# Kernel optimization log

Hardware: AMD Instinct MI355X
Metric: run time of the kernel (lower is better)

The kernel has to match this reference:

```python
import jax, jax.numpy as jnp
import numpy as np

B_, C_, H_, W_, N_ = 2, 256, 64, 64, 16


def setup_inputs() -> dict:
    key = jax.random.key(0)
    ks = jax.random.split(key, 6)
    return {
        "features": jax.random.normal(ks[0], (B_, C_, H_, W_), jnp.float32),
        "A_log": jax.random.normal(ks[1], (C_, N_), jnp.float32) * 0.5,
        "D": jax.random.normal(ks[2], (C_,), jnp.float32),
        "W_delta": jax.random.normal(ks[3], (C_, C_), jnp.float32) * 0.02,
        "b_delta": jnp.zeros((C_,), jnp.float32),
        "W_B": jax.random.normal(ks[4], (C_, N_), jnp.float32) * 0.02,
        "W_C": jax.random.normal(ks[5], (C_, N_), jnp.float32) * 0.02,
    }


def _selective_scan(x, A_log, D, W_delta, b_delta, W_B, W_C):
    # x: (B, L, C) -> (B, L, C). Canonical S6 selective scan (mamba corrector).
    delta = jax.nn.softplus(x @ W_delta + b_delta)          # (B, L, C)
    Bm = x @ W_B                                            # (B, L, N)
    Cm = x @ W_C                                            # (B, L, N)
    A = -jnp.exp(A_log)                                     # (C, N), negative real
    dA = jnp.exp(delta[..., None] * A)                      # (B, L, C, N)
    dBx = (delta * x)[..., None] * Bm[:, :, None, :]        # (B, L, C, N)

    def combine(left, right):
        a_l, b_l = left
        a_r, b_r = right
        return (a_l * a_r, a_r * b_l + b_r)

    # h_t = dA_t * h_{t-1} + dBx_t, computed in parallel over L
    _, h = jax.lax.associative_scan(combine, (dA, dBx), axis=1)
    y = jnp.einsum('blcn,bln->blc', h, Cm) + x * D          # (B, L, C)
    return y


def reference(features, A_log, D, W_delta, b_delta, W_B, W_C):
    B, C, H, W = features.shape
    corr = lambda x: _selective_scan(x, A_log, D, W_delta, b_delta, W_B, W_C)

    # direction 1: row-major forward
    flat = features.reshape(B, C, H * W).transpose(0, 2, 1)        # (B, HW, C)
    out1 = corr(flat)
    # direction 2: row-major reversed
    out2 = jnp.flip(corr(jnp.flip(flat, axis=1)), axis=1)
    # direction 3: rows flipped vertically (flip over H), scan, flip back
    rows = features.transpose(0, 2, 3, 1)                          # (B, H, W, C)
    rows_f = jnp.flip(rows, axis=1).reshape(B, H * W, C)
    out3 = jnp.flip(corr(rows_f).reshape(B, H, W, C), axis=1).reshape(B, H * W, C)
    # direction 4: column-major, flipped over W, scan, flip + transpose back
    cols = features.transpose(0, 3, 2, 1)                          # (B, W, H, C)
    cols_f = jnp.flip(cols, axis=1).reshape(B, W * H, C)
    out4 = jnp.flip(corr(cols_f).reshape(B, W, H, C), axis=1)
    out4 = out4.transpose(0, 2, 1, 3).reshape(B, H * W, C)

    mamba_out = (out1 + out2 + out3 + out4) / 4                    # (B, HW, C)
    return mamba_out.transpose(0, 2, 1).reshape(B, C, H, W)
```

## Files before the change

### kernel.cpp

```cpp
#include <hip/hip_runtime.h>
#include <cstdint>
#include <cstddef>

#define BB 2
#define CC 256
#define NN 16
#define LL 4096
#define NCH 128
#define CLEN 32
#define LOG2E 1.4426950408889634f

typedef __attribute__((ext_vector_type(8))) short short8;
typedef __attribute__((ext_vector_type(4))) float f32x4;

__device__ __forceinline__ float softplus_f(float z) {
    return fmaxf(z, 0.f) + log1pf(expf(-fabsf(z)));
}

__device__ __forceinline__ uint32_t pack_bf2(float d, float u) {
    uint32_t lo = (__float_as_uint(d) + 0x8000u) >> 16;
    uint32_t hh = (__float_as_uint(u) + 0x8000u) & 0xffff0000u;
    return hh | lo;
}

__device__ __forceinline__ short bf16r(float f) {
    return (short)((__float_as_uint(f) + 0x8000u) >> 16);
}

__global__ __launch_bounds__(256) void k1_mfma(
    const float* __restrict__ feat, const float* __restrict__ Wd,
    const float* __restrict__ bd, const float* __restrict__ WB,
    const float* __restrict__ WC, uint32_t* __restrict__ du,
    float* __restrict__ Bm, float* __restrict__ Cm)
{
    int blk = blockIdx.x;
    int b  = blk >> 9;
    int lt = (blk >> 2) & 127;
    int ct = blk & 3;
    int l0 = lt * 32, c0 = ct * 64;
    const float* fbase = feat + (size_t)b * CC * LL;
    int t    = threadIdx.x;
    int lane = t & 63;
    int wq   = t >> 6;
    int m    = lane & 15;
    int quad = lane >> 4;
    int m0   = (wq & 1) * 16;
    int n0   = (wq >> 1) * 32;
    bool doBC = (ct == 0);

    __shared__ __align__(16) short sA[32][264];
    __shared__ __align__(16) short sB[64][264];
    __shared__ __align__(16) short sWB[16][264];
    __shared__ __align__(16) short sWC[16][264];

    #pragma unroll
    for (int p = 0; p < 8; ++p) {
        int k  = p * 32 + (t >> 3);
        int lc = (t & 7) * 4;
        f32x4 v = *(const f32x4*)&fbase[(size_t)k * LL + l0 + lc];
        #pragma unroll
        for (int i = 0; i < 4; ++i) sA[lc + i][k] = bf16r(v[i]);
    }
    #pragma unroll
    for (int p = 0; p < 16; ++p) {
        int k  = p * 16 + (t >> 4);
        int cc = (t & 15) * 4;
        f32x4 v = *(const f32x4*)&Wd[(size_t)k * CC + c0 + cc];
        #pragma unroll
        for (int i = 0; i < 4; ++i) sB[cc + i][k] = bf16r(v[i]);
    }
    if (doBC) {
        #pragma unroll
        for (int p = 0; p < 4; ++p) {
            int k  = p * 64 + (t >> 2);
            int nc = (t & 3) * 4;
            f32x4 vb = *(const f32x4*)&WB[(size_t)k * NN + nc];
            f32x4 vc = *(const f32x4*)&WC[(size_t)k * NN + nc];
            #pragma unroll
            for (int i = 0; i < 4; ++i) {
                sWB[nc + i][k] = bf16r(vb[i]);
                sWC[nc + i][k] = bf16r(vc[i]);
            }
        }
    }
    __syncthreads();

    f32x4 acc0 = {0.f, 0.f, 0.f, 0.f};
    f32x4 acc1 = {0.f, 0.f, 0.f, 0.f};
    f32x4 accB = {0.f, 0.f, 0.f, 0.f};
    const short (*sWsel)[264] = (wq >> 1) ? sWC : sWB;

    for (int ks = 0; ks < 8; ++ks) {
        int k8 = ks * 32 + quad * 8;
        short8 af  = *(const short8*)&sA[m0 + m][k8];
        short8 bf0 = *(const short8*)&sB[n0 + m][k8];
        short8 bf1 = *(const short8*)&sB[n0 + 16 + m][k8];
        acc0 = __builtin_amdgcn_mfma_f32_16x16x32_bf16(af, bf0, acc0, 0, 0, 0);
        acc1 = __builtin_amdgcn_mfma_f32_16x16x32_bf16(af, bf1, acc1, 0, 0, 0);
        if (doBC) {
            short8 bbf = *(const short8*)&sWsel[m][k8];
            accB = __builtin_amdgcn_mfma_f32_16x16x32_bf16(af, bbf, accB, 0, 0, 0);
        }
    }

    if (doBC) {
        float* dst = (wq >> 1) ? Cm : Bm;
        #pragma unroll
        for (int r = 0; r < 4; ++r) {
            int l = l0 + m0 + quad * 4 + r;
            dst[((size_t)b * LL + l) * NN + m] = accB[r];
        }
    }

    float bd0 = bd[c0 + n0 + m];
    float bd1 = bd[c0 + n0 + 16 + m];
    int cA = c0 + n0 + m;
    int cB = cA + 16;
    int lb = l0 + m0 + quad * 4;
    f32x4 xv0 = *(const f32x4*)&fbase[(size_t)cA * LL + lb];
    f32x4 xv1 = *(const f32x4*)&fbase[(size_t)cB * LL + lb];
    #pragma unroll
    for (int r = 0; r < 4; ++r) {
        float d0 = softplus_f(acc0[r] + bd0);
        float d1 = softplus_f(acc1[r] + bd1);
        du[((size_t)b * LL + lb + r) * CC + cA] = pack_bf2(d0, d0 * xv0[r]);
        du[((size_t)b * LL + lb + r) * CC + cB] = pack_bf2(d1, d1 * xv1[r]);
    }
}

__global__ __launch_bounds__(256) void p1_aggr(
    const uint32_t* __restrict__ du, const float* __restrict__ Bm,
    const float* __restrict__ A_log, float* __restrict__ P, float* __restrict__ S)
{
    int blk = blockIdx.x;
    int b  = (blk >> 7) & 1;
    int ch = blk & 127;
    int c = threadIdx.x;
    __shared__ float sBm[CLEN * NN];
    __shared__ uint32_t sW[CLEN * 256];

    float A2[NN];
    {
        const float4* al = (const float4*)(A_log + c * NN);
        #pragma unroll
        for (int q = 0; q < 4; ++q) {
            float4 v = al[q];
            A2[q*4+0] = -expf(v.x) * LOG2E;
            A2[q*4+1] = -expf(v.y) * LOG2E;
            A2[q*4+2] = -expf(v.z) * LOG2E;
            A2[q*4+3] = -expf(v.w) * LOG2E;
        }
    }

    if (blk < 256) {
        int p0 = 32 * ch;
        for (int i = threadIdx.x; i < CLEN * NN; i += 256) {
            int j = i >> 4, nn = i & 15;
            sBm[i] = Bm[((size_t)b * LL + (p0 + j)) * NN + nn];
        }
        const uint32_t* dub = du + (size_t)b * LL * CC + c;
        {
            uint32_t wt[CLEN];
            #pragma unroll
            for (int j = 0; j < CLEN; ++j) wt[j] = dub[(size_t)(p0 + j) * CC];
            #pragma unroll
            for (int j = 0; j < CLEN; ++j) sW[j * 256 + c] = wt[j];
        }
        __syncthreads();
        float Sf[NN] = {}, Sr[NN] = {}, pref[NN];
        #pragma unroll
        for (int nn = 0; nn < NN; ++nn) pref[nn] = 1.f;
        float sumd = 0.f;
        #pragma unroll 1
        for (int j = 0; j < CLEN; ++j) {
            uint32_t wj = sW[j * 256 + c];
            float dx = __uint_as_float(wj << 16);
            float uy = __uint_as_float(wj & 0xffff0000u);
            sumd += dx;
            float dA[NN];
            #pragma unroll
            for (int nn = 0; nn < NN; ++nn) dA[nn] = __builtin_amdgcn_exp2f(A2[nn] * dx);
            #pragma unroll
            for (int nn = 0; nn < NN; ++nn) {
                float Bu = uy * sBm[j * 16 + nn];
                Sf[nn] = fmaf(dA[nn], Sf[nn], Bu);
                Sr[nn] = fmaf(pref[nn], Bu, Sr[nn]);
                pref[nn] *= dA[nn];
            }
        }
        size_t base0 = ((size_t)(b * 128 + ch)) * 4096 + (size_t)c * 16;
        size_t base1 = ((size_t)((2 + b) * 128 + (127 - ch))) * 4096 + (size_t)c * 16;
        #pragma unroll
        for (int nn = 0; nn < NN; ++nn) {
            P[base0 + nn] = __builtin_amdgcn_exp2f(A2[nn] * sumd);
            S[base0 + nn] = Sf[nn];
            S[base1 + nn] = Sr[nn];
        }
    } else {
        int p0 = 63 - (ch >> 1) + 2048 * (ch & 1);
        const int inner = 64;
        for (int i = threadIdx.x; i < CLEN * NN; i += 256) {
            int j = i >> 4, nn = i & 15;
            sBm[i] = Bm[((size_t)b * LL + (p0 + inner * j)) * NN + nn];
        }
        const uint32_t* dub = du + (size_t)b * LL * CC + c;
        {
            uint32_t wt[CLEN];
            #pragma unroll
            for (int j = 0; j < CLEN; ++j) wt[j] = dub[(size_t)(p0 + inner * j) * CC];
            #pragma unroll
            for (int j = 0; j < CLEN; ++j) sW[j * 256 + c] = wt[j];
        }
        __syncthreads();
        float Sv[NN] = {};
        float sumd = 0.f;
        #pragma unroll 1
        for (int j = 0; j < CLEN; ++j) {
            uint32_t wj = sW[j * 256 + c];
            float dx = __uint_as_float(wj << 16);
            float uy = __uint_as_float(wj & 0xffff0000u);
            sumd += dx;
            float dA[NN];
            #pragma unroll
            for (int nn = 0; nn < NN; ++nn) dA[nn] = __builtin_amdgcn_exp2f(A2[nn] * dx);
            #pragma unroll
            for (int nn = 0; nn < NN; ++nn)
                Sv[nn] = fmaf(dA[nn], Sv[nn], uy * sBm[j * 16 + nn]);
        }
        size_t base = ((size_t)((4 + b) * 128 + ch)) * 4096 + (size_t)c * 16;
        #pragma unroll
        for (int nn = 0; nn < NN; ++nn) {
            P[base + nn] = __builtin_amdgcn_exp2f(A2[nn] * sumd);
            S[base + nn] = Sv[nn];
        }
    }
}

__global__ __launch_bounds__(128) void p2_scan(
    const float* __restrict__ P, const float* __restrict__ S, float* __restrict__ Hin)
{
    int r = blockIdx.x * 128 + threadIdx.x;
    int cn = r & 4095;
    int db = r >> 12;
    int d = db >> 1;
    int cls = (d == 1) ? 1 : ((d == 3) ? 2 : 0);
    int b = db & 1;
    const size_t sbase = ((size_t)(cls * 2 + b) * 128) * 4096 + cn;
    const size_t pbase = (d == 1) ? (((size_t)b * 128) * 4096 + cn) : sbase;
    const size_t obase = ((size_t)db * 128) * 4096 + cn;
    float h = 0.f;
    for (int g = 0; g < 16; ++g) {
        float pv[8], sv[8];
        #pragma unroll
        for (int i = 0; i < 8; ++i) {
            int ch = g * 8 + i;
            int chm = (d == 2) ? (126 - 2 * (ch >> 1) + (ch & 1)) : ch;
            int chp = (d == 1) ? (127 - ch) : chm;
            pv[i] = P[pbase + (size_t)chp * 4096];
            sv[i] = S[sbase + (size_t)chm * 4096];
        }
        #pragma unroll
        for (int i = 0; i < 8; ++i) {
            Hin[obase + (size_t)(g * 8 + i) * 4096] = h;
            h = fmaf(pv[i], h, sv[i]);
        }
    }
}

__global__ __launch_bounds__(256) void p3_replay(
    const uint32_t* __restrict__ du, const float* __restrict__ Bm,
    const float* __restrict__ Cm, const float* __restrict__ A_log,
    const float* __restrict__ Hin, float* __restrict__ yAB,
    float* __restrict__ yC)
{
    int blk = blockIdx.x;
    int b  = (blk >> 7) & 1;
    int ch = blk & 127;
    int c = threadIdx.x;
    __shared__ float sBm[CLEN * NN];
    __shared__ float sCm[CLEN * NN];
    __shared__ uint32_t sW[CLEN * 256];
    __shared__ float sY[CLEN * 256];

    float A2[NN];
    {
        const float4* al = (const float4*)(A_log + c * NN);
        #pragma unroll
        for (int q = 0; q < 4; ++q) {
            float4 v = al[q];
            A2[q*4+0] = -expf(v.x) * LOG2E;
            A2[q*4+1] = -expf(v.y) * LOG2E;
            A2[q*4+2] = -expf(v.z) * LOG2E;
            A2[q*4+3] = -expf(v.w) * LOG2E;
        }
    }

    if (blk < 256) {
        int p0 = 32 * ch;
        for (int i = threadIdx.x; i < CLEN * NN; i += 256) {
            int j = i >> 4, nn = i & 15;
            size_t o = ((size_t)b * LL + (p0 + j)) * NN + nn;
            sBm[i] = Bm[o];
            sCm[i] = Cm[o];
        }
        const uint32_t* dub = du + (size_t)b * LL * CC + c;
        {
            uint32_t wt[CLEN];
            #pragma unroll
            for (int j = 0; j < CLEN; ++j) wt[j] = dub[(size_t)(p0 + j) * CC];
            #pragma unroll
            for (int j = 0; j < CLEN; ++j) sW[j * 256 + c] = wt[j];
        }

        int chr = 127 - ch;
        float h1[NN];
        {
            const float4* hp1 = (const float4*)(Hin + ((size_t)(1 * 2 + b) * 128 + chr) * 4096 + (size_t)c * 16);
            #pragma unroll
            for (int q = 0; q < 4; ++q) {
                float4 v1 = hp1[q];
                h1[q*4+0]=v1.x; h1[q*4+1]=v1.y; h1[q*4+2]=v1.z; h1[q*4+3]=v1.w;
            }
        }
        __syncthreads();
        #pragma unroll 1
        for (int j = CLEN - 1; j >= 0; --j) {
            uint32_t wj = sW[j * 256 + c];
            float dx = __uint_as_float(wj << 16);
            float uy = __uint_as_float(wj & 0xffff0000u);
            float dA[NN];
            #pragma unroll
            for (int nn = 0; nn < NN; ++nn) dA[nn] = __builtin_amdgcn_exp2f(A2[nn] * dx);
            float yv = 0.f;
            #pragma unroll
            for (int nn = 0; nn < NN; ++nn) {
                float Bu = uy * sBm[j * 16 + nn];
                h1[nn] = fmaf(dA[nn], h1[nn], Bu);
                yv = fmaf(h1[nn], sCm[j * 16 + nn], yv);
            }
            sY[j * 256 + c] = yv;
        }

        int ch2 = 126 - (ch & ~1) + (ch & 1);
        float h0[NN], h2[NN];
        {
            const float4* hp0 = (const float4*)(Hin + ((size_t)(0 * 2 + b) * 128 + ch)  * 4096 + (size_t)c * 16);
            const float4* hp2 = (const float4*)(Hin + ((size_t)(2 * 2 + b) * 128 + ch2) * 4096 + (size_t)c * 16);
            #pragma unroll
            for (int q = 0; q < 4; ++q) {
                float4 v0 = hp0[q], v2 = hp2[q];
                h0[q*4+0]=v0.x; h0[q*4+1]=v0.y; h0[q*4+2]=v0.z; h0[q*4+3]=v0.w;
                h2[q*4+0]=v2.x; h2[q*4+1]=v2.y; h2[q*4+2]=v2.z; h2[q*4+3]=v2.w;
            }
        }
        #pragma unroll 1
        for (int j = 0; j < CLEN; ++j) {
            uint32_t wj = sW[j * 256 + c];
            float dx = __uint_as_float(wj << 16);
            float uy = __uint_as_float(wj & 0xffff0000u);
            float dA[NN];
            #pragma unroll
            for (int nn = 0; nn < NN; ++nn) dA[nn] = __builtin_amdgcn_exp2f(A2[nn] * dx);
            float y0v = 0.f, y2v = 0.f;
            #pragma unroll
            for (int nn = 0; nn < NN; ++nn) {
                float Bu = uy * sBm[j * 16 + nn];
                float cm = sCm[j * 16 + nn];
                h0[nn] = fmaf(dA[nn], h0[nn], Bu);
                h2[nn] = fmaf(dA[nn], h2[nn], Bu);
                y0v = fmaf(h0[nn], cm, y0v);
                y2v = fmaf(h2[nn], cm, y2v);
            }
            yAB[((size_t)b * LL + p0 + j) * CC + c] = 0.25f * (y0v + y2v + sY[j * 256 + c]);
        }
    } else {
        int p0 = 63 - (ch >> 1) + 2048 * (ch & 1);
        const int inner = 64;
        for (int i = threadIdx.x; i < CLEN * NN; i += 256) {
            int j = i >> 4, nn = i & 15;
            size_t o = ((size_t)b * LL + (p0 + inner * j)) * NN + nn;
            sBm[i] = Bm[o];
            sCm[i] = Cm[o];
        }
        const uint32_t* dub = du + (size_t)b * LL * CC + c;
        {
            uint32_t wt[CLEN];
            #pragma unroll
            for (int j = 0; j < CLEN; ++j) wt[j] = dub[(size_t)(p0 + inner * j) * CC];
            #pragma unroll
            for (int j = 0; j < CLEN; ++j) sW[j * 256 + c] = wt[j];
        }
        float h[NN];
        {
            const float4* hp = (const float4*)(Hin + ((size_t)(3 * 2 + b) * 128 + ch) * 4096 + (size_t)c * 16);
            #pragma unroll
            for (int q = 0; q < 4; ++q) {
                float4 v = hp[q];
                h[q*4+0]=v.x; h[q*4+1]=v.y; h[q*4+2]=v.z; h[q*4+3]=v.w;
            }
        }
        __syncthreads();
        #pragma unroll 1
        for (int j = 0; j < CLEN; ++j) {
            uint32_t wj = sW[j * 256 + c];
            float dx = __uint_as_float(wj << 16);
            float uy = __uint_as_float(wj & 0xffff0000u);
            float dA[NN];
            #pragma unroll
            for (int nn = 0; nn < NN; ++nn) dA[nn] = __builtin_amdgcn_exp2f(A2[nn] * dx);
            float yv = 0.f;
            #pragma unroll
            for (int nn = 0; nn < NN; ++nn) {
                float Bu = uy * sBm[j * 16 + nn];
                h[nn] = fmaf(dA[nn], h[nn], Bu);
                yv = fmaf(h[nn], sCm[j * 16 + nn], yv);
            }
            yC[((size_t)b * LL + p0 + inner * j) * CC + c] = 0.25f * yv;
        }
    }
}

__global__ __launch_bounds__(256) void k6_reduce(
    const float* __restrict__ feat, const float* __restrict__ D,
    const float* __restrict__ yAB, const float* __restrict__ yC,
    float* __restrict__ out)
{
    int pt = blockIdx.x & 63;
    int ct = (blockIdx.x >> 6) & 3;
    int b  = blockIdx.x >> 8;
    int p0 = pt * 64, c0 = ct * 64;
    __shared__ float tile[64 * 65];
    {
        int cl = threadIdx.x & 63;
        int pg = threadIdx.x >> 6;
        #pragma unroll
        for (int pp = 0; pp < 16; ++pp) {
            int pl = pp * 4 + pg;
            size_t ix = ((size_t)b * LL + p0 + pl) * CC + c0 + cl;
            tile[cl * 65 + pl] = yAB[ix] + yC[ix];
        }
    }
    __syncthreads();
    {
        int pl = threadIdx.x & 63;
        int cg = threadIdx.x >> 6;
        #pragma unroll
        for (int cc = 0; cc < 16; ++cc) {
            int cloc = cc * 4 + cg;
            int c = c0 + cloc;
            size_t o = ((size_t)b * CC + c) * LL + p0 + pl;
            out[o] = tile[cloc * 65 + pl] + feat[o] * D[c];
        }
    }
}

extern "C" void kernel_launch(void* const* d_in, const int* in_sizes, int n_in,
                              void* d_out, int out_size, void* d_ws, size_t ws_size,
                              hipStream_t stream)
{
    const float* feat  = (const float*)d_in[0];
    const float* A_log = (const float*)d_in[1];
    const float* D     = (const float*)d_in[2];
    const float* Wd    = (const float*)d_in[3];
    const float* bd    = (const float*)d_in[4];
    const float* WB    = (const float*)d_in[5];
    const float* WC    = (const float*)d_in[6];
    float* out = (float*)d_out;

    float* ws  = (float*)d_ws;
    uint32_t* du = (uint32_t*)ws;
    float* Bm  = ws  + (size_t)2097152;
    float* Cm  = Bm  + (size_t)131072;
    float* P   = Cm  + (size_t)131072;
    float* S   = P   + (size_t)3145728;
    float* Hin = S   + (size_t)3145728;
    float* yAB = Hin + (size_t)4194304;
    float* yC  = yAB + (size_t)2097152;

    k1_mfma<<<1024, 256, 0, stream>>>(feat, Wd, bd, WB, WC, du, Bm, Cm);
    p1_aggr<<<512, 256, 0, stream>>>(du, Bm, A_log, P, S);
    p2_scan<<<256, 128, 0, stream>>>(P, S, Hin);
    p3_replay<<<512, 256, 0, stream>>>(du, Bm, Cm, A_log, Hin, yAB, yC);
    k6_reduce<<<512, 256, 0, stream>>>(feat, D, yAB, yC, out);
}
```

Baseline: 153.5 us.

## Fuse all five stages into one persistent kernel with grid barriers

Replaces the five separate launches (projection GEMM, chunk aggregation, inter-chunk scan, replay, reduce) with a single persistent kernel of 512 blocks. The stages are separated by atomic-counter grid barriers, with a memset to reset the counters before launch. The aggregation and replay stages now reuse the same shared-memory chunk data, so the du/Bm/Cm reload in the replay stage is removed. The aim is to remove launch gaps and the redundant reload. In exchange, all 512 blocks must be co-resident to avoid deadlock, the spin barriers add their own cost, and the scan stage uses only part of the grid.

```diff
diff --git a/kernel.cpp b/kernel.cpp
--- a/kernel.cpp
+++ b/kernel.cpp
@@ -2,12 +2,11 @@
 #include <cstdint>
 #include <cstddef>
 
-#define BB 2
 #define CC 256
 #define NN 16
 #define LL 4096
-#define NCH 128
 #define CLEN 32
+#define NBLK 512
 #define LOG2E 1.4426950408889634f
 
 typedef __attribute__((ext_vector_type(8))) short short8;
@@ -27,18 +26,37 @@
     return (short)((__float_as_uint(f) + 0x8000u) >> 16);
 }
 
-__global__ __launch_bounds__(256) void k1_mfma(
-    const float* __restrict__ feat, const float* __restrict__ Wd,
+__device__ __forceinline__ void gbar(uint32_t* cnt) {
+    __syncthreads();
+    if (threadIdx.x == 0) {
+        __threadfence();
+        atomicAdd(cnt, 1u);
+        int spins = 0;
+        while (atomicAdd(cnt, 0u) < (uint32_t)NBLK) {
+            __builtin_amdgcn_s_sleep(16);
+            if (++spins > (1 << 26)) break;
+        }
+        __threadfence();
+    }
+    __syncthreads();
+}
+
+union Smem {
+    struct { short A[32][264]; short B[64][264]; short WB[16][264]; short WC[16][264]; } k1;
+    struct { float bm[CLEN * NN]; float cm[CLEN * NN]; uint32_t w[CLEN * 256]; float y[CLEN * 256]; } ps;
+    float tile[64 * 65];
+};
+
+__global__ __launch_bounds__(256, 2) void fused_all(
+    const float* __restrict__ feat, const float* __restrict__ A_log,
+    const float* __restrict__ Dv, const float* __restrict__ Wd,
     const float* __restrict__ bd, const float* __restrict__ WB,
-    const float* __restrict__ WC, uint32_t* __restrict__ du,
-    float* __restrict__ Bm, float* __restrict__ Cm)
+    const float* __restrict__ WC, float* __restrict__ out,
+    uint32_t* __restrict__ du, float* __restrict__ Bm, float* __restrict__ Cm,
+    float* __restrict__ P, float* __restrict__ S, float* __restrict__ Hin,
+    float* __restrict__ yAB, float* __restrict__ yC, uint32_t* __restrict__ bar)
 {
-    int blk = blockIdx.x;
-    int b  = blk >> 9;
-    int lt = (blk >> 2) & 127;
-    int ct = blk & 3;
-    int l0 = lt * 32, c0 = ct * 64;
-    const float* fbase = feat + (size_t)b * CC * LL;
+    __shared__ Smem sm;
     int t    = threadIdx.x;
     int lane = t & 63;
     int wq   = t >> 6;
@@ -46,99 +64,92 @@
     int quad = lane >> 4;
     int m0   = (wq & 1) * 16;
     int n0   = (wq >> 1) * 32;
-    bool doBC = (ct == 0);
-
-    __shared__ __align__(16) short sA[32][264];
-    __shared__ __align__(16) short sB[64][264];
-    __shared__ __align__(16) short sWB[16][264];
-    __shared__ __align__(16) short sWC[16][264];
-
-    #pragma unroll
-    for (int p = 0; p < 8; ++p) {
-        int k  = p * 32 + (t >> 3);
-        int lc = (t & 7) * 4;
-        f32x4 v = *(const f32x4*)&fbase[(size_t)k * LL + l0 + lc];
-        #pragma unroll
-        for (int i = 0; i < 4; ++i) sA[lc + i][k] = bf16r(v[i]);
-    }
-    #pragma unroll
-    for (int p = 0; p < 16; ++p) {
-        int k  = p * 16 + (t >> 4);
-        int cc = (t & 15) * 4;
-        f32x4 v = *(const f32x4*)&Wd[(size_t)k * CC + c0 + cc];
-        #pragma unroll
-        for (int i = 0; i < 4; ++i) sB[cc + i][k] = bf16r(v[i]);
-    }
-    if (doBC) {
-        #pragma unroll
-        for (int p = 0; p < 4; ++p) {
-            int k  = p * 64 + (t >> 2);
-            int nc = (t & 3) * 4;
-            f32x4 vb = *(const f32x4*)&WB[(size_t)k * NN + nc];
-            f32x4 vc = *(const f32x4*)&WC[(size_t)k * NN + nc];
-            #pragma unroll
-            for (int i = 0; i < 4; ++i) {
-                sWB[nc + i][k] = bf16r(vb[i]);
-                sWC[nc + i][k] = bf16r(vc[i]);
-            }
-        }
-    }
-    __syncthreads();
-
-    f32x4 acc0 = {0.f, 0.f, 0.f, 0.f};
-    f32x4 acc1 = {0.f, 0.f, 0.f, 0.f};
-    f32x4 accB = {0.f, 0.f, 0.f, 0.f};
-    const short (*sWsel)[264] = (wq >> 1) ? sWC : sWB;
-
-    for (int ks = 0; ks < 8; ++ks) {
-        int k8 = ks * 32 + quad * 8;
-        short8 af  = *(const short8*)&sA[m0 + m][k8];
-        short8 bf0 = *(const short8*)&sB[n0 + m][k8];
-        short8 bf1 = *(const short8*)&sB[n0 + 16 + m][k8];
-        acc0 = __builtin_amdgcn_mfma_f32_16x16x32_bf16(af, bf0, acc0, 0, 0, 0);
-        acc1 = __builtin_amdgcn_mfma_f32_16x16x32_bf16(af, bf1, acc1, 0, 0, 0);
+
+    for (int it = 0; it < 2; ++it) {
+        __syncthreads();
+        int blk = it * 512 + blockIdx.x;
+        int b  = blk >> 9;
+        int lt = (blk >> 2) & 127;
+        int ct = blk & 3;
+        int l0 = lt * 32, c0 = ct * 64;
+        const float* fbase = feat + (size_t)b * CC * LL;
+        bool doBC = (ct == 0);
+
+        #pragma unroll
+        for (int p = 0; p < 8; ++p) {
+            int k  = p * 32 + (t >> 3);
+            int lc = (t & 7) * 4;
+            f32x4 v = *(const f32x4*)&fbase[(size_t)k * LL + l0 + lc];
+            #pragma unroll
+            for (int i = 0; i < 4; ++i) sm.k1.A[lc + i][k] = bf16r(v[i]);
+        }
+        #pragma unroll
+        for (int p = 0; p < 16; ++p) {
+            int k  = p * 16 + (t >> 4);
+            int cc = (t & 15) * 4;
+            f32x4 v = *(const f32x4*)&Wd[(size_t)k * CC + c0 + cc];
+            #pragma unroll
+            for (int i = 0; i < 4; ++i) sm.k1.B[cc + i][k] = bf16r(v[i]);
+        }
         if (doBC) {
-            short8 bbf = *(const short8*)&sWsel[m][k8];
-            accB = __builtin_amdgcn_mfma_f32_16x16x32_bf16(af, bbf, accB, 0, 0, 0);
-        }
-    }
-
-    if (doBC) {
-        float* dst = (wq >> 1) ? Cm : Bm;
+            #pragma unroll
+            for (int p = 0; p < 4; ++p) {
+                int k  = p * 64 + (t >> 2);
+                int nc = (t & 3) * 4;
+                f32x4 vb = *(const f32x4*)&WB[(size_t)k * NN + nc];
+                f32x4 vc = *(const f32x4*)&WC[(size_t)k * NN + nc];
+                #pragma unroll
+                for (int i = 0; i < 4; ++i) {
+                    sm.k1.WB[nc + i][k] = bf16r(vb[i]);
+                    sm.k1.WC[nc + i][k] = bf16r(vc[i]);
+                }
+            }
+        }
+        __syncthreads();
+
+        f32x4 acc0 = {0.f, 0.f, 0.f, 0.f};
+        f32x4 acc1 = {0.f, 0.f, 0.f, 0.f};
+        f32x4 accB = {0.f, 0.f, 0.f, 0.f};
+        const short (*sWsel)[264] = (wq >> 1) ? sm.k1.WC : sm.k1.WB;
+        for (int ks = 0; ks < 8; ++ks) {
+            int k8 = ks * 32 + quad * 8;
+            short8 af  = *(const short8*)&sm.k1.A[m0 + m][k8];
+            short8 bf0 = *(const short8*)&sm.k1.B[n0 + m][k8];
+            short8 bf1 = *(const short8*)&sm.k1.B[n0 + 16 + m][k8];
+            acc0 = __builtin_amdgcn_mfma_f32_16x16x32_bf16(af, bf0, acc0, 0, 0, 0);
+            acc1 = __builtin_amdgcn_mfma_f32_16x16x32_bf16(af, bf1, acc1, 0, 0, 0);
+            if (doBC) {
+                short8 bbf = *(const short8*)&sWsel[m][k8];
+                accB = __builtin_amdgcn_mfma_f32_16x16x32_bf16(af, bbf, accB, 0, 0, 0);
+            }
+        }
+        if (doBC) {
+            float* dst = (wq >> 1) ? Cm : Bm;
+            #pragma unroll
+            for (int r = 0; r < 4; ++r) {
+                int l = l0 + m0 + quad * 4 + r;
+                dst[((size_t)b * LL + l) * NN + m] = accB[r];
+            }
+        }
+        float bd0 = bd[c0 + n0 + m];
+        float bd1 = bd[c0 + n0 + 16 + m];
+        int cA = c0 + n0 + m;
+        int cB = cA + 16;
+        int lb = l0 + m0 + quad * 4;
+        f32x4 xv0 = *(const f32x4*)&fbase[(size_t)cA * LL + lb];
+        f32x4 xv1 = *(const f32x4*)&fbase[(size_t)cB * LL + lb];
         #pragma unroll
         for (int r = 0; r < 4; ++r) {
-            int l = l0 + m0 + quad * 4 + r;
-            dst[((size_t)b * LL + l) * NN + m] = accB[r];
-        }
-    }
-
-    float bd0 = bd[c0 + n0 + m];
-    float bd1 = bd[c0 + n0 + 16 + m];
-    int cA = c0 + n0 + m;
-    int cB = cA + 16;
-    int lb = l0 + m0 + quad * 4;
-    f32x4 xv0 = *(const f32x4*)&fbase[(size_t)cA * LL + lb];
-    f32x4 xv1 = *(const f32x4*)&fbase[(size_t)cB * LL + lb];
-    #pragma unroll
-    for (int r = 0; r < 4; ++r) {
-        float d0 = softplus_f(acc0[r] + bd0);
-        float d1 = softplus_f(acc1[r] + bd1);
-        du[((size_t)b * LL + lb + r) * CC + cA] = pack_bf2(d0, d0 * xv0[r]);
-        du[((size_t)b * LL + lb + r) * CC + cB] = pack_bf2(d1, d1 * xv1[r]);
-    }
-}
-
-__global__ __launch_bounds__(256) void p1_aggr(
-    const uint32_t* __restrict__ du, const float* __restrict__ Bm,
-    const float* __restrict__ A_log, float* __restrict__ P, float* __restrict__ S)
-{
-    int blk = blockIdx.x;
-    int b  = (blk >> 7) & 1;
-    int ch = blk & 127;
-    int c = threadIdx.x;
-    __shared__ float sBm[CLEN * NN];
-    __shared__ uint32_t sW[CLEN * 256];
-
+            float d0 = softplus_f(acc0[r] + bd0);
+            float d1 = softplus_f(acc1[r] + bd1);
+            du[((size_t)b * LL + lb + r) * CC + cA] = pack_bf2(d0, d0 * xv0[r]);
+            du[((size_t)b * LL + lb + r) * CC + cB] = pack_bf2(d1, d1 * xv1[r]);
+        }
+    }
+
+    gbar(bar + 0);
+
+    int c = t;
     float A2[NN];
     {
         const float4* al = (const float4*)(A_log + c * NN);
@@ -152,28 +163,38 @@
         }
     }
 
-    if (blk < 256) {
-        int p0 = 32 * ch;
-        for (int i = threadIdx.x; i < CLEN * NN; i += 256) {
-            int j = i >> 4, nn = i & 15;
-            sBm[i] = Bm[((size_t)b * LL + (p0 + j)) * NN + nn];
-        }
-        const uint32_t* dub = du + (size_t)b * LL * CC + c;
-        {
-            uint32_t wt[CLEN];
-            #pragma unroll
-            for (int j = 0; j < CLEN; ++j) wt[j] = dub[(size_t)(p0 + j) * CC];
-            #pragma unroll
-            for (int j = 0; j < CLEN; ++j) sW[j * 256 + c] = wt[j];
-        }
-        __syncthreads();
+    int blk = blockIdx.x;
+    int b1  = (blk >> 7) & 1;
+    int ch  = blk & 127;
+    bool isRow = (blk < 256);
+    int p0, inner;
+    if (isRow) { p0 = 32 * ch;                              inner = 1;  }
+    else       { p0 = 63 - (ch >> 1) + 2048 * (ch & 1);     inner = 64; }
+
+    for (int i = t; i < CLEN * NN; i += 256) {
+        int j = i >> 4, nn = i & 15;
+        size_t o = ((size_t)b1 * LL + (p0 + inner * j)) * NN + nn;
+        sm.ps.bm[i] = Bm[o];
+        sm.ps.cm[i] = Cm[o];
+    }
+    {
+        const uint32_t* dub = du + (size_t)b1 * LL * CC + c;
+        uint32_t wt[CLEN];
+        #pragma unroll
+        for (int j = 0; j < CLEN; ++j) wt[j] = dub[(size_t)(p0 + inner * j) * CC];
+        #pragma unroll
+        for (int j = 0; j < CLEN; ++j) sm.ps.w[j * 256 + c] = wt[j];
+    }
+    __syncthreads();
+
+    if (isRow) {
         float Sf[NN] = {}, Sr[NN] = {}, pref[NN];
         #pragma unroll
         for (int nn = 0; nn < NN; ++nn) pref[nn] = 1.f;
         float sumd = 0.f;
         #pragma unroll 1
         for (int j = 0; j < CLEN; ++j) {
-            uint32_t wj = sW[j * 256 + c];
+            uint32_t wj = sm.ps.w[j * 256 + c];
             float dx = __uint_as_float(wj << 16);
             float uy = __uint_as_float(wj & 0xffff0000u);
             sumd += dx;
@@ -182,14 +203,14 @@
             for (int nn = 0; nn < NN; ++nn) dA[nn] = __builtin_amdgcn_exp2f(A2[nn] * dx);
             #pragma unroll
             for (int nn = 0; nn < NN; ++nn) {
-                float Bu = uy * sBm[j * 16 + nn];
+                float Bu = uy * sm.ps.bm[j * 16 + nn];
                 Sf[nn] = fmaf(dA[nn], Sf[nn], Bu);
                 Sr[nn] = fmaf(pref[nn], Bu, Sr[nn]);
                 pref[nn] *= dA[nn];
             }
         }
-        size_t base0 = ((size_t)(b * 128 + ch)) * 4096 + (size_t)c * 16;
-        size_t base1 = ((size_t)((2 + b) * 128 + (127 - ch))) * 4096 + (size_t)c * 16;
+        size_t base0 = ((size_t)(b1 * 128 + ch)) * 4096 + (size_t)c * 16;
+        size_t base1 = ((size_t)((2 + b1) * 128 + (127 - ch))) * 4096 + (size_t)c * 16;
         #pragma unroll
         for (int nn = 0; nn < NN; ++nn) {
             P[base0 + nn] = __builtin_amdgcn_exp2f(A2[nn] * sumd);
@@ -197,26 +218,11 @@
             S[base1 + nn] = Sr[nn];
         }
     } else {
-        int p0 = 63 - (ch >> 1) + 2048 * (ch & 1);
-        const int inner = 64;
-        for (int i = threadIdx.x; i < CLEN * NN; i += 256) {
-            int j = i >> 4, nn = i & 15;
-            sBm[i] = Bm[((size_t)b * LL + (p0 + inner * j)) * NN + nn];
-        }
-        const uint32_t* dub = du + (size_t)b * LL * CC + c;
-        {
-            uint32_t wt[CLEN];
-            #pragma unroll
-            for (int j = 0; j < CLEN; ++j) wt[j] = dub[(size_t)(p0 + inner * j) * CC];
-            #pragma unroll
-            for (int j = 0; j < CLEN; ++j) sW[j * 256 + c] = wt[j];
-        }
-        __syncthreads();
         float Sv[NN] = {};
         float sumd = 0.f;
         #pragma unroll 1
         for (int j = 0; j < CLEN; ++j) {
-            uint32_t wj = sW[j * 256 + c];
+            uint32_t wj = sm.ps.w[j * 256 + c];
             float dx = __uint_as_float(wj << 16);
             float uy = __uint_as_float(wj & 0xffff0000u);
             sumd += dx;
@@ -225,107 +231,65 @@
             for (int nn = 0; nn < NN; ++nn) dA[nn] = __builtin_amdgcn_exp2f(A2[nn] * dx);
             #pragma unroll
             for (int nn = 0; nn < NN; ++nn)
-                Sv[nn] = fmaf(dA[nn], Sv[nn], uy * sBm[j * 16 + nn]);
-        }
-        size_t base = ((size_t)((4 + b) * 128 + ch)) * 4096 + (size_t)c * 16;
+                Sv[nn] = fmaf(dA[nn], Sv[nn], uy * sm.ps.bm[j * 16 + nn]);
+        }
+        size_t base = ((size_t)((4 + b1) * 128 + ch)) * 4096 + (size_t)c * 16;
         #pragma unroll
         for (int nn = 0; nn < NN; ++nn) {
             P[base + nn] = __builtin_amdgcn_exp2f(A2[nn] * sumd);
             S[base + nn] = Sv[nn];
         }
     }
-}
-
-__global__ __launch_bounds__(128) void p2_scan(
-    const float* __restrict__ P, const float* __restrict__ S, float* __restrict__ Hin)
-{
-    int r = blockIdx.x * 128 + threadIdx.x;
-    int cn = r & 4095;
-    int db = r >> 12;
-    int d = db >> 1;
-    int cls = (d == 1) ? 1 : ((d == 3) ? 2 : 0);
-    int b = db & 1;
-    const size_t sbase = ((size_t)(cls * 2 + b) * 128) * 4096 + cn;
-    const size_t pbase = (d == 1) ? (((size_t)b * 128) * 4096 + cn) : sbase;
-    const size_t obase = ((size_t)db * 128) * 4096 + cn;
-    float h = 0.f;
-    for (int g = 0; g < 16; ++g) {
-        float pv[8], sv[8];
-        #pragma unroll
-        for (int i = 0; i < 8; ++i) {
-            int ch = g * 8 + i;
-            int chm = (d == 2) ? (126 - 2 * (ch >> 1) + (ch & 1)) : ch;
-            int chp = (d == 1) ? (127 - ch) : chm;
-            pv[i] = P[pbase + (size_t)chp * 4096];
-            sv[i] = S[sbase + (size_t)chm * 4096];
-        }
-        #pragma unroll
-        for (int i = 0; i < 8; ++i) {
-            Hin[obase + (size_t)(g * 8 + i) * 4096] = h;
-            h = fmaf(pv[i], h, sv[i]);
-        }
-    }
-}
-
-__global__ __launch_bounds__(256) void p3_replay(
-    const uint32_t* __restrict__ du, const float* __restrict__ Bm,
-    const float* __restrict__ Cm, const float* __restrict__ A_log,
-    const float* __restrict__ Hin, float* __restrict__ yAB,
-    float* __restrict__ yC)
-{
-    int blk = blockIdx.x;
-    int b  = (blk >> 7) & 1;
-    int ch = blk & 127;
-    int c = threadIdx.x;
-    __shared__ float sBm[CLEN * NN];
-    __shared__ float sCm[CLEN * NN];
-    __shared__ uint32_t sW[CLEN * 256];
-    __shared__ float sY[CLEN * 256];
-
-    float A2[NN];
+
+    gbar(bar + 1);
+
     {
-        const float4* al = (const float4*)(A_log + c * NN);
-        #pragma unroll
-        for (int q = 0; q < 4; ++q) {
-            float4 v = al[q];
-            A2[q*4+0] = -expf(v.x) * LOG2E;
-            A2[q*4+1] = -expf(v.y) * LOG2E;
-            A2[q*4+2] = -expf(v.z) * LOG2E;
-            A2[q*4+3] = -expf(v.w) * LOG2E;
-        }
-    }
-
-    if (blk < 256) {
-        int p0 = 32 * ch;
-        for (int i = threadIdx.x; i < CLEN * NN; i += 256) {
-            int j = i >> 4, nn = i & 15;
-            size_t o = ((size_t)b * LL + (p0 + j)) * NN + nn;
-            sBm[i] = Bm[o];
-            sCm[i] = Cm[o];
-        }
-        const uint32_t* dub = du + (size_t)b * LL * CC + c;
-        {
-            uint32_t wt[CLEN];
-            #pragma unroll
-            for (int j = 0; j < CLEN; ++j) wt[j] = dub[(size_t)(p0 + j) * CC];
-            #pragma unroll
-            for (int j = 0; j < CLEN; ++j) sW[j * 256 + c] = wt[j];
-        }
-
+        int gid = blockIdx.x * 256 + t;
+        if (gid < 32768) {
+            int cn = gid & 4095;
+            int db = gid >> 12;
+            int d = db >> 1;
+            int cls = (d == 1) ? 1 : ((d == 3) ? 2 : 0);
+            int bb = db & 1;
+            const size_t sbase = ((size_t)(cls * 2 + bb) * 128) * 4096 + cn;
+            const size_t pbase = (d == 1) ? (((size_t)bb * 128) * 4096 + cn) : sbase;
+            const size_t obase = ((size_t)db * 128) * 4096 + cn;
+            float h = 0.f;
+            for (int g = 0; g < 16; ++g) {
+                float pv[8], sv[8];
+                #pragma unroll
+                for (int i = 0; i < 8; ++i) {
+                    int cc = g * 8 + i;
+                    int chm = (d == 2) ? (126 - 2 * (cc >> 1) + (cc & 1)) : cc;
+                    int chp = (d == 1) ? (127 - cc) : chm;
+                    pv[i] = P[pbase + (size_t)chp * 4096];
+                    sv[i] = S[sbase + (size_t)chm * 4096];
+                }
+                #pragma unroll
+                for (int i = 0; i < 8; ++i) {
+                    Hin[obase + (size_t)(g * 8 + i) * 4096] = h;
+                    h = fmaf(pv[i], h, sv[i]);
+                }
+            }
+        }
+    }
+
+    gbar(bar + 2);
+
+    if (isRow) {
         int chr = 127 - ch;
         float h1[NN];
         {
-            const float4* hp1 = (const float4*)(Hin + ((size_t)(1 * 2 + b) * 128 + chr) * 4096 + (size_t)c * 16);
+            const float4* hp1 = (const float4*)(Hin + ((size_t)(1 * 2 + b1) * 128 + chr) * 4096 + (size_t)c * 16);
             #pragma unroll
             for (int q = 0; q < 4; ++q) {
                 float4 v1 = hp1[q];
                 h1[q*4+0]=v1.x; h1[q*4+1]=v1.y; h1[q*4+2]=v1.z; h1[q*4+3]=v1.w;
             }
         }
-        __syncthreads();
         #pragma unroll 1
         for (int j = CLEN - 1; j >= 0; --j) {
-            uint32_t wj = sW[j * 256 + c];
+            uint32_t wj = sm.ps.w[j * 256 + c];
             float dx = __uint_as_float(wj << 16);
             float uy = __uint_as_float(wj & 0xffff0000u);
             float dA[NN];
@@ -334,18 +298,17 @@
             float yv = 0.f;
             #pragma unroll
             for (int nn = 0; nn < NN; ++nn) {
-                float Bu = uy * sBm[j * 16 + nn];
+                float Bu = uy * sm.ps.bm[j * 16 + nn];
                 h1[nn] = fmaf(dA[nn], h1[nn], Bu);
-                yv = fmaf(h1[nn], sCm[j * 16 + nn], yv);
-            }
-            sY[j * 256 + c] = yv;
-        }
-
+                yv = fmaf(h1[nn], sm.ps.cm[j * 16 + nn], yv);
+            }
+            sm.ps.y[j * 256 + c] = yv;
+        }
         int ch2 = 126 - (ch & ~1) + (ch & 1);
         float h0[NN], h2[NN];
         {
-            const float4* hp0 = (const float4*)(Hin + ((size_t)(0 * 2 + b) * 128 + ch)  * 4096 + (size_t)c * 16);
-            const float4* hp2 = (const float4*)(Hin + ((size_t)(2 * 2 + b) * 128 + ch2) * 4096 + (size_t)c * 16);
+            const float4* hp0 = (const float4*)(Hin + ((size_t)(0 * 2 + b1) * 128 + ch)  * 4096 + (size_t)c * 16);
+            const float4* hp2 = (const float4*)(Hin + ((size_t)(2 * 2 + b1) * 128 + ch2) * 4096 + (size_t)c * 16);
             #pragma unroll
             for (int q = 0; q < 4; ++q) {
                 float4 v0 = hp0[q], v2 = hp2[q];
@@ -355,7 +318,7 @@
         }
         #pragma unroll 1
         for (int j = 0; j < CLEN; ++j) {
-            uint32_t wj = sW[j * 256 + c];
+            uint32_t wj = sm.ps.w[j * 256 + c];
             float dx = __uint_as_float(wj << 16);
             float uy = __uint_as_float(wj & 0xffff0000u);
             float dA[NN];
@@ -364,45 +327,28 @@
             float y0v = 0.f, y2v = 0.f;
             #pragma unroll
             for (int nn = 0; nn < NN; ++nn) {
-                float Bu = uy * sBm[j * 16 + nn];
-                float cm = sCm[j * 16 + nn];
+                float Bu = uy * sm.ps.bm[j * 16 + nn];
+                float cm = sm.ps.cm[j * 16 + nn];
                 h0[nn] = fmaf(dA[nn], h0[nn], Bu);
                 h2[nn] = fmaf(dA[nn], h2[nn], Bu);
                 y0v = fmaf(h0[nn], cm, y0v);
                 y2v = fmaf(h2[nn], cm, y2v);
             }
-            yAB[((size_t)b * LL + p0 + j) * CC + c] = 0.25f * (y0v + y2v + sY[j * 256 + c]);
+            yAB[((size_t)b1 * LL + p0 + j) * CC + c] = 0.25f * (y0v + y2v + sm.ps.y[j * 256 + c]);
         }
     } else {
-        int p0 = 63 - (ch >> 1) + 2048 * (ch & 1);
-        const int inner = 64;
-        for (int i = threadIdx.x; i < CLEN * NN; i += 256) {
-            int j = i >> 4, nn = i & 15;
-            size_t o = ((size_t)b * LL + (p0 + inner * j)) * NN + nn;
-            sBm[i] = Bm[o];
-            sCm[i] = Cm[o];
-        }
-        const uint32_t* dub = du + (size_t)b * LL * CC + c;
-        {
-            uint32_t wt[CLEN];
-            #pragma unroll
-            for (int j = 0; j < CLEN; ++j) wt[j] = dub[(size_t)(p0 + inner * j) * CC];
-            #pragma unroll
-            for (int j = 0; j < CLEN; ++j) sW[j * 256 + c] = wt[j];
-        }
         float h[NN];
         {
-            const float4* hp = (const float4*)(Hin + ((size_t)(3 * 2 + b) * 128 + ch) * 4096 + (size_t)c * 16);
+            const float4* hp = (const float4*)(Hin + ((size_t)(3 * 2 + b1) * 128 + ch) * 4096 + (size_t)c * 16);
             #pragma unroll
             for (int q = 0; q < 4; ++q) {
                 float4 v = hp[q];
                 h[q*4+0]=v.x; h[q*4+1]=v.y; h[q*4+2]=v.z; h[q*4+3]=v.w;
             }
         }
-        __syncthreads();
         #pragma unroll 1
         for (int j = 0; j < CLEN; ++j) {
-            uint32_t wj = sW[j * 256 + c];
+            uint32_t wj = sm.ps.w[j * 256 + c];
             float dx = __uint_as_float(wj << 16);
             float uy = __uint_as_float(wj & 0xffff0000u);
             float dA[NN];
@@ -411,45 +357,42 @@
             float yv = 0.f;
             #pragma unroll
             for (int nn = 0; nn < NN; ++nn) {
-                float Bu = uy * sBm[j * 16 + nn];
+                float Bu = uy * sm.ps.bm[j * 16 + nn];
                 h[nn] = fmaf(dA[nn], h[nn], Bu);
-                yv = fmaf(h[nn], sCm[j * 16 + nn], yv);
-            }
-            yC[((size_t)b * LL + p0 + inner * j) * CC + c] = 0.25f * yv;
-        }
-    }
-}
-
-__global__ __launch_bounds__(256) void k6_reduce(
-    const float* __restrict__ feat, const float* __restrict__ D,
-    const float* __restrict__ yAB, const float* __restrict__ yC,
-    float* __restrict__ out)
-{
-    int pt = blockIdx.x & 63;
-    int ct = (blockIdx.x >> 6) & 3;
-    int b  = blockIdx.x >> 8;
-    int p0 = pt * 64, c0 = ct * 64;
-    __shared__ float tile[64 * 65];
+                yv = fmaf(h[nn], sm.ps.cm[j * 16 + nn], yv);
+            }
+            yC[((size_t)b1 * LL + p0 + inner * j) * CC + c] = 0.25f * yv;
+        }
+    }
+
+    gbar(bar + 3);
+
     {
-        int cl = threadIdx.x & 63;
-        int pg = threadIdx.x >> 6;
-        #pragma unroll
-        for (int pp = 0; pp < 16; ++pp) {
-            int pl = pp * 4 + pg;
-            size_t ix = ((size_t)b * LL + p0 + pl) * CC + c0 + cl;
-            tile[cl * 65 + pl] = yAB[ix] + yC[ix];
-        }
-    }
-    __syncthreads();
-    {
-        int pl = threadIdx.x & 63;
-        int cg = threadIdx.x >> 6;
-        #pragma unroll
-        for (int cc = 0; cc < 16; ++cc) {
-            int cloc = cc * 4 + cg;
-            int c = c0 + cloc;
-            size_t o = ((size_t)b * CC + c) * LL + p0 + pl;
-            out[o] = tile[cloc * 65 + pl] + feat[o] * D[c];
+        int pt  = blockIdx.x & 63;
+        int ct6 = (blockIdx.x >> 6) & 3;
+        int b6  = blockIdx.x >> 8;
+        int p06 = pt * 64, c06 = ct6 * 64;
+        {
+            int cl = t & 63;
+            int pg = t >> 6;
+            #pragma unroll
+            for (int pp = 0; pp < 16; ++pp) {
+                int pl = pp * 4 + pg;
+                size_t ix = ((size_t)b6 * LL + p06 + pl) * CC + c06 + cl;
+                sm.tile[cl * 65 + pl] = yAB[ix] + yC[ix];
+            }
+        }
+        __syncthreads();
+        {
+            int pl = t & 63;
+            int cg6 = t >> 6;
+            #pragma unroll
+            for (int cc = 0; cc < 16; ++cc) {
+                int cloc = cc * 4 + cg6;
+                int c6 = c06 + cloc;
+                size_t o = ((size_t)b6 * CC + c6) * LL + p06 + pl;
+                out[o] = sm.tile[cloc * 65 + pl] + feat[o] * Dv[c6];
+            }
         }
     }
 }
@@ -460,7 +403,7 @@
 {
     const float* feat  = (const float*)d_in[0];
     const float* A_log = (const float*)d_in[1];
-    const float* D     = (const float*)d_in[2];
+    const float* Dv    = (const float*)d_in[2];
     const float* Wd    = (const float*)d_in[3];
     const float* bd    = (const float*)d_in[4];
     const float* WB    = (const float*)d_in[5];
@@ -476,10 +419,11 @@
     float* Hin = S   + (size_t)3145728;
     float* yAB = Hin + (size_t)4194304;
     float* yC  = yAB + (size_t)2097152;
-
-    k1_mfma<<<1024, 256, 0, stream>>>(feat, Wd, bd, WB, WC, du, Bm, Cm);
-    p1_aggr<<<512, 256, 0, stream>>>(du, Bm, A_log, P, S);
-    p2_scan<<<256, 128, 0, stream>>>(P, S, Hin);
-    p3_replay<<<512, 256, 0, stream>>>(du, Bm, Cm, A_log, Hin, yAB, yC);
-    k6_reduce<<<512, 256, 0, stream>>>(feat, D, yAB, yC, out);
-}
+    uint32_t* bar = (uint32_t*)(yC + (size_t)2097152);
+
+    hipMemsetAsync(bar, 0, 4 * sizeof(uint32_t), stream);
+
+    fused_all<<<NBLK, 256, 0, stream>>>(
+        feat, A_log, Dv, Wd, bd, WB, WC, out,
+        du, Bm, Cm, P, S, Hin, yAB, yC, bar);
+}
```

Result: slower. 365.4 us (+138.1%).
